# Optimization experiments

Measured on AMD Instinct MI355X. Metric: run time of the kernel, lower is better.

## Reference

```python
import jax, jax.numpy as jnp
import numpy as np

B, IN, H = 4096, 512, 1024
ALPHA, RHO = 0.001, 0.05

def setup_inputs() -> dict:
    key = jax.random.key(0)
    ks = jax.random.split(key, 9)
    inp = jax.random.normal(ks[0], (B, IN), dtype=jnp.float32)
    time = jax.random.uniform(ks[1], (B, 1), dtype=jnp.float32) * 100.0
    hx = jax.random.normal(ks[2], (B, H), dtype=jnp.float32)
    cx = jax.random.normal(ks[3], (B, H), dtype=jnp.float32)
    # params (match torch init scales loosely)
    Wxh_w = jax.random.normal(ks[4], (4 * H, IN), dtype=jnp.float32) / np.sqrt(IN)
    Wxh_b = jnp.zeros((4 * H,), dtype=jnp.float32)
    Whh_w = jax.random.normal(ks[5], (4 * H, H), dtype=jnp.float32) / np.sqrt(H)
    tau = jax.random.normal(ks[6], (H,), dtype=jnp.float32) * 0.5 + 5.0
    s = jax.random.uniform(ks[7], (H,), dtype=jnp.float32) * tau
    alpha = jnp.array([ALPHA], dtype=jnp.float32)
    rho = jnp.array([RHO], dtype=jnp.float32)
    return {"input": inp, "time": time, "hx": hx, "cx": cx,
            "Wxh_w": Wxh_w, "Wxh_b": Wxh_b, "Whh_w": Whh_w,
            "tau": tau, "s": s, "alpha": alpha, "rho": rho}

def _time_gate(time, s, tau, alpha, rho):
    # phi: [B, H] (time [B,1] broadcast against s/tau [H])
    phi = jnp.fmod(time - s, tau) / tau
    k = jnp.where(phi < rho / 2.0, 2.0 * phi / rho,
        jnp.where(phi < rho, 2.0 - 2.0 * phi / rho, alpha * phi))
    # computed under torch.no_grad() in the original
    return jax.lax.stop_gradient(k)

def reference(input, time, hx, cx, Wxh_w, Wxh_b, Whh_w, tau, s, alpha, rho):
    gates = input @ Wxh_w.T + Wxh_b + hx @ Whh_w.T  # [B, 4H]
    i, f, g, o = jnp.split(gates, 4, axis=1)
    k = _time_gate(time, s, tau, alpha, rho)
    ft = jax.nn.sigmoid(f + 1.0 - k)
    it = jax.nn.sigmoid(i) * k
    gt = jnp.tanh(g) * k
    ot = jax.nn.sigmoid(o) * k
    cy = ft * cx + it * gt
    hy = ot * jnp.tanh(cy)
    return (hy, cy)
```

## Files before the change

### kernel.cpp

```cpp
#include <hip/hip_runtime.h>
#include <hip/hip_bf16.h>

#define AS1 __attribute__((address_space(1)))
#define AS3 __attribute__((address_space(3)))

typedef _Float16 half_t;
typedef __attribute__((ext_vector_type(8))) _Float16 f16x8;
typedef __attribute__((ext_vector_type(4))) float f32x4;

static constexpr int Bsz = 4096;
static constexpr int INs = 512;
static constexpr int Hs  = 1024;
static constexpr int BM  = 128;
static constexpr int BH  = 32;
static constexpr int BK  = 64;

static constexpr size_t XN  = (size_t)Bsz * INs;
static constexpr size_t HXN = (size_t)Bsz * Hs;
static constexpr size_t WXN = (size_t)4 * Hs * INs;
static constexpr size_t WHN = (size_t)4 * Hs * Hs;
static constexpr size_t OFF_X  = 0;
static constexpr size_t OFF_HX = XN;
static constexpr size_t OFF_WX = XN + HXN;
static constexpr size_t OFF_WH = XN + HXN + WXN;
static constexpr size_t TOT    = XN + HXN + WXN + WHN;

__global__ __launch_bounds__(256)
void cvt_kernel(const float* __restrict__ x, const float* __restrict__ hx,
                const float* __restrict__ wx, const float* __restrict__ wh,
                half_t* __restrict__ ws) {
  const size_t nthr = (size_t)gridDim.x * blockDim.x;
  for (size_t i8 = (size_t)blockIdx.x * blockDim.x + threadIdx.x;
       i8 < TOT / 8; i8 += nthr) {
    const size_t e = i8 * 8;
    const float* src; size_t off;
    if (e < OFF_HX)      { src = x;  off = e - OFF_X; }
    else if (e < OFF_WX) { src = hx; off = e - OFF_HX; }
    else if (e < OFF_WH) { src = wx; off = e - OFF_WX; }
    else                 { src = wh; off = e - OFF_WH; }
    const f32x4 a = *(const f32x4*)(src + off);
    const f32x4 b = *(const f32x4*)(src + off + 4);
    f16x8 o;
    o[0] = (half_t)a[0]; o[1] = (half_t)a[1]; o[2] = (half_t)a[2]; o[3] = (half_t)a[3];
    o[4] = (half_t)b[0]; o[5] = (half_t)b[1]; o[6] = (half_t)b[2]; o[7] = (half_t)b[3];
    *(f16x8*)(ws + e) = o;
  }
}

template <bool FROMWS>
__global__ __launch_bounds__(256, 2)
void plstm_gemm(const void* __restrict__ xin_,
                const float* __restrict__ timep,
                const void* __restrict__ hxp_,
                const float* __restrict__ cxp,
                const void* __restrict__ wxh_,
                const float* __restrict__ biasp,
                const void* __restrict__ whh_,
                const float* __restrict__ taup,
                const float* __restrict__ sp,
                const float* __restrict__ alphap,
                const float* __restrict__ rhop,
                float* __restrict__ outp)
{
  __shared__ half_t As[BM * BK];
  __shared__ half_t Bs[BM * BK];

  const int tid  = threadIdx.x;
  const int w    = tid >> 6;
  const int lane = tid & 63;
  const int l15  = lane & 15;
  const int grp  = lane >> 4;

  const int m0 = blockIdx.x * BM;
  const int h0 = blockIdx.y * BH;

  f32x4 acc[2][8] = {};

  const int ldr = tid >> 3;
  const int ldc = tid & 7;

  for (int phase = 0; phase < 2; ++phase) {
    const void* Ap = (phase == 0) ? xin_ : hxp_;
    const void* Wp = (phase == 0) ? wxh_ : whh_;
    const int Ka = (phase == 0) ? INs : Hs;

    for (int k0 = 0; k0 < Ka; k0 += BK) {
      #pragma unroll
      for (int i = 0; i < 4; ++i) {
        const int e    = i * 32 + ldr;
        const int gc8  = ldc ^ (e & 7);
        const int wrow = (e >> 5) * Hs + h0 + (e & 31);
        if (FROMWS) {
          const half_t* ga = (const half_t*)Ap + (size_t)(m0 + e) * Ka + (k0 + gc8 * 8);
          __builtin_amdgcn_global_load_lds((AS1 void*)ga,
                                           (AS3 void*)(As + (e * 8 + ldc) * 8), 16, 0, 0);
          const half_t* gw = (const half_t*)Wp + (size_t)wrow * Ka + (k0 + gc8 * 8);
          __builtin_amdgcn_global_load_lds((AS1 void*)gw,
                                           (AS3 void*)(Bs + (e * 8 + ldc) * 8), 16, 0, 0);
        } else {
          const float* ga = (const float*)Ap + (size_t)(m0 + e) * Ka + (k0 + gc8 * 8);
          const f32x4 a0 = *(const f32x4*)ga, a1 = *(const f32x4*)(ga + 4);
          f16x8 pa;
          pa[0]=(half_t)a0[0]; pa[1]=(half_t)a0[1]; pa[2]=(half_t)a0[2]; pa[3]=(half_t)a0[3];
          pa[4]=(half_t)a1[0]; pa[5]=(half_t)a1[1]; pa[6]=(half_t)a1[2]; pa[7]=(half_t)a1[3];
          *(f16x8*)(As + (e * 8 + ldc) * 8) = pa;
          const float* gw = (const float*)Wp + (size_t)wrow * Ka + (k0 + gc8 * 8);
          const f32x4 b0 = *(const f32x4*)gw, b1 = *(const f32x4*)(gw + 4);
          f16x8 pb;
          pb[0]=(half_t)b0[0]; pb[1]=(half_t)b0[1]; pb[2]=(half_t)b0[2]; pb[3]=(half_t)b0[3];
          pb[4]=(half_t)b1[0]; pb[5]=(half_t)b1[1]; pb[6]=(half_t)b1[2]; pb[7]=(half_t)b1[3];
          *(f16x8*)(Bs + (e * 8 + ldc) * 8) = pb;
        }
      }
      __syncthreads();

      #pragma unroll
      for (int kk = 0; kk < 2; ++kk) {
        const int c8 = (kk * 4 + grp) ^ (l15 & 7);
        f16x8 af[2], bfr[8];
        #pragma unroll
        for (int mt = 0; mt < 2; ++mt) {
          const int e = w * 32 + mt * 16 + l15;
          af[mt] = *(const f16x8*)(As + (e * 8 + c8) * 8);
        }
        #pragma unroll
        for (int nt = 0; nt < 8; ++nt) {
          const int e = nt * 16 + l15;
          bfr[nt] = *(const f16x8*)(Bs + (e * 8 + c8) * 8);
        }
        #pragma unroll
        for (int mt = 0; mt < 2; ++mt)
          #pragma unroll
          for (int nt = 0; nt < 8; ++nt)
            acc[mt][nt] = __builtin_amdgcn_mfma_f32_16x16x32_f16(
                af[mt], bfr[nt], acc[mt][nt], 0, 0, 0);
      }
      __syncthreads();
    }
  }

  const float alphav = alphap[0];
  const float rhov   = rhop[0];
  const float rho_half = rhov * 0.5f;

  float sv[2], tauv[2], bi[2], bff[2], bg[2], bo[2];
  #pragma unroll
  for (int nt2 = 0; nt2 < 2; ++nt2) {
    const int h = h0 + nt2 * 16 + l15;
    sv[nt2]   = sp[h];
    tauv[nt2] = taup[h];
    bi[nt2]   = biasp[h];
    bff[nt2]  = biasp[Hs + h];
    bg[nt2]   = biasp[2 * Hs + h];
    bo[nt2]   = biasp[3 * Hs + h];
  }

  #pragma unroll
  for (int mt = 0; mt < 2; ++mt) {
    #pragma unroll
    for (int r = 0; r < 4; ++r) {
      const int brow = m0 + w * 32 + mt * 16 + grp * 4 + r;
      const float timev = timep[brow];
      #pragma unroll
      for (int nt2 = 0; nt2 < 2; ++nt2) {
        const int h = h0 + nt2 * 16 + l15;
        const float iv = acc[mt][0 + nt2][r] + bi[nt2];
        const float fv = acc[mt][2 + nt2][r] + bff[nt2];
        const float gv = acc[mt][4 + nt2][r] + bg[nt2];
        const float ov = acc[mt][6 + nt2][r] + bo[nt2];

        const float phi = fmodf(timev - sv[nt2], tauv[nt2]) / tauv[nt2];
        float kv;
        if (phi < rho_half)      kv = (2.0f * phi) / rhov;
        else if (phi < rhov)     kv = 2.0f - (2.0f * phi) / rhov;
        else                     kv = alphav * phi;

        const float cxv = cxp[(size_t)brow * Hs + h];
        const float ft = 1.0f / (1.0f + expf(-(fv + 1.0f - kv)));
        const float it = kv / (1.0f + expf(-iv));
        const float gt = tanhf(gv) * kv;
        const float ot = kv / (1.0f + expf(-ov));
        const float cy = ft * cxv + it * gt;
        const float hy = ot * tanhf(cy);

        outp[(size_t)brow * Hs + h] = hy;
        outp[(size_t)Bsz * Hs + (size_t)brow * Hs + h] = cy;
      }
    }
  }
}

extern "C" void kernel_launch(void* const* d_in, const int* in_sizes, int n_in,
                              void* d_out, int out_size, void* d_ws, size_t ws_size,
                              hipStream_t stream) {
  (void)in_sizes; (void)n_in; (void)out_size;
  const float* xin   = (const float*)d_in[0];
  const float* timep = (const float*)d_in[1];
  const float* hxp   = (const float*)d_in[2];
  const float* cxp   = (const float*)d_in[3];
  const float* wxh   = (const float*)d_in[4];
  const float* biasp = (const float*)d_in[5];
  const float* whh   = (const float*)d_in[6];
  const float* taup  = (const float*)d_in[7];
  const float* sp    = (const float*)d_in[8];
  const float* alphap= (const float*)d_in[9];
  const float* rhop  = (const float*)d_in[10];
  float* outp = (float*)d_out;

  dim3 grid(Bsz / BM, Hs / BH);
  if (ws_size >= TOT * sizeof(half_t)) {
    half_t* ws = (half_t*)d_ws;
    cvt_kernel<<<2048, 256, 0, stream>>>(xin, hxp, wxh, whh, ws);
    plstm_gemm<true><<<grid, 256, 0, stream>>>(
        ws + OFF_X, timep, ws + OFF_HX, cxp, ws + OFF_WX, biasp, ws + OFF_WH,
        taup, sp, alphap, rhop, outp);
  } else {
    plstm_gemm<false><<<grid, 256, 0, stream>>>(
        xin, timep, hxp, cxp, wxh, biasp, whh,
        taup, sp, alphap, rhop, outp);
  }
}
```

Measured before the change: 203.2 us.

## Rebalance warp tiling, precompute time gate in convert kernel, use fast transcendentals

```diff
diff --git a/kernel.cpp b/kernel.cpp
--- a/kernel.cpp
+++ b/kernel.cpp
@@ -1,5 +1,4 @@
 #include <hip/hip_runtime.h>
-#include <hip/hip_bf16.h>
 
 #define AS1 __attribute__((address_space(1)))
 #define AS3 __attribute__((address_space(3)))
@@ -24,15 +23,26 @@
 static constexpr size_t OFF_WX = XN + HXN;
 static constexpr size_t OFF_WH = XN + HXN + WXN;
 static constexpr size_t TOT    = XN + HXN + WXN + WHN;
+static constexpr size_t KN     = (size_t)Bsz * Hs;
+
+__device__ __forceinline__ float sigm(float x) {
+  return 1.0f / (1.0f + __expf(-x));
+}
+__device__ __forceinline__ float tanh_fast(float x) {
+  const float e = __expf(2.0f * x);
+  return 1.0f - 2.0f / (e + 1.0f);
+}
 
 __global__ __launch_bounds__(256)
 void cvt_kernel(const float* __restrict__ x, const float* __restrict__ hx,
                 const float* __restrict__ wx, const float* __restrict__ wh,
-                half_t* __restrict__ ws) {
-  const size_t nthr = (size_t)gridDim.x * blockDim.x;
-  for (size_t i8 = (size_t)blockIdx.x * blockDim.x + threadIdx.x;
-       i8 < TOT / 8; i8 += nthr) {
-    const size_t e = i8 * 8;
+                const float* __restrict__ timep, const float* __restrict__ sp,
+                const float* __restrict__ taup, const float* __restrict__ alphap,
+                const float* __restrict__ rhop,
+                half_t* __restrict__ ws, float* __restrict__ kout) {
+  const size_t cid = (size_t)blockIdx.x * 256 + threadIdx.x;
+  if (cid < TOT / 8) {
+    const size_t e = cid * 8;
     const float* src; size_t off;
     if (e < OFF_HX)      { src = x;  off = e - OFF_X; }
     else if (e < OFF_WX) { src = hx; off = e - OFF_HX; }
@@ -41,14 +51,38 @@
     const f32x4 a = *(const f32x4*)(src + off);
     const f32x4 b = *(const f32x4*)(src + off + 4);
     f16x8 o;
-    o[0] = (half_t)a[0]; o[1] = (half_t)a[1]; o[2] = (half_t)a[2]; o[3] = (half_t)a[3];
-    o[4] = (half_t)b[0]; o[5] = (half_t)b[1]; o[6] = (half_t)b[2]; o[7] = (half_t)b[3];
+    o[0]=(half_t)a[0]; o[1]=(half_t)a[1]; o[2]=(half_t)a[2]; o[3]=(half_t)a[3];
+    o[4]=(half_t)b[0]; o[5]=(half_t)b[1]; o[6]=(half_t)b[2]; o[7]=(half_t)b[3];
     *(f16x8*)(ws + e) = o;
-  }
-}
-
-template <bool FROMWS>
-__global__ __launch_bounds__(256, 2)
+  } else {
+    const size_t e2 = (cid - TOT / 8) * 8;
+    const int b = (int)(e2 >> 10);
+    const int h = (int)(e2 & 1023);
+    const float tv = timep[b];
+    const float alphav = alphap[0];
+    const float rhov   = rhop[0];
+    const float rh     = 0.5f * rhov;
+    const f32x4 s0 = *(const f32x4*)(sp + h),   s1 = *(const f32x4*)(sp + h + 4);
+    const f32x4 t0 = *(const f32x4*)(taup + h), t1 = *(const f32x4*)(taup + h + 4);
+    f32x4 k0, k1;
+    #pragma unroll
+    for (int j = 0; j < 8; ++j) {
+      const float sv   = j < 4 ? s0[j] : s1[j - 4];
+      const float tauv = j < 4 ? t0[j] : t1[j - 4];
+      const float phi = fmodf(tv - sv, tauv) / tauv;
+      float kv;
+      if (phi < rh)        kv = (2.0f * phi) / rhov;
+      else if (phi < rhov) kv = 2.0f - (2.0f * phi) / rhov;
+      else                 kv = alphav * phi;
+      if (j < 4) k0[j] = kv; else k1[j - 4] = kv;
+    }
+    *(f32x4*)(kout + e2) = k0;
+    *(f32x4*)(kout + e2 + 4) = k1;
+  }
+}
+
+template <int MODE>
+__global__ __launch_bounds__(256, 3)
 void plstm_gemm(const void* __restrict__ xin_,
                 const float* __restrict__ timep,
                 const void* __restrict__ hxp_,
@@ -60,6 +94,7 @@
                 const float* __restrict__ sp,
                 const float* __restrict__ alphap,
                 const float* __restrict__ rhop,
+                const float* __restrict__ kp,
                 float* __restrict__ outp)
 {
   __shared__ half_t As[BM * BK];
@@ -70,11 +105,13 @@
   const int lane = tid & 63;
   const int l15  = lane & 15;
   const int grp  = lane >> 4;
+  const int wr   = w >> 1;
+  const int wc   = w & 1;
 
   const int m0 = blockIdx.x * BM;
   const int h0 = blockIdx.y * BH;
 
-  f32x4 acc[2][8] = {};
+  f32x4 acc[4][4] = {};
 
   const int ldr = tid >> 3;
   const int ldc = tid & 7;
@@ -89,8 +126,8 @@
       for (int i = 0; i < 4; ++i) {
         const int e    = i * 32 + ldr;
         const int gc8  = ldc ^ (e & 7);
-        const int wrow = (e >> 5) * Hs + h0 + (e & 31);
-        if (FROMWS) {
+        const int wrow = ((e >> 4) & 3) * Hs + h0 + ((e >> 6) << 4) + (e & 15);
+        if (MODE >= 1) {
           const half_t* ga = (const half_t*)Ap + (size_t)(m0 + e) * Ka + (k0 + gc8 * 8);
           __builtin_amdgcn_global_load_lds((AS1 void*)ga,
                                            (AS3 void*)(As + (e * 8 + ldc) * 8), 16, 0, 0);
@@ -116,22 +153,22 @@
 
       #pragma unroll
       for (int kk = 0; kk < 2; ++kk) {
-        const int c8 = (kk * 4 + grp) ^ (l15 & 7);
-        f16x8 af[2], bfr[8];
+        const int c8x = (kk * 4 + grp);
+        f16x8 af[4], bfr[4];
         #pragma unroll
-        for (int mt = 0; mt < 2; ++mt) {
-          const int e = w * 32 + mt * 16 + l15;
-          af[mt] = *(const f16x8*)(As + (e * 8 + c8) * 8);
+        for (int mt = 0; mt < 4; ++mt) {
+          const int e = wr * 64 + mt * 16 + l15;
+          af[mt] = *(const f16x8*)(As + (e * 8 + (c8x ^ (l15 & 7))) * 8);
         }
         #pragma unroll
-        for (int nt = 0; nt < 8; ++nt) {
-          const int e = nt * 16 + l15;
-          bfr[nt] = *(const f16x8*)(Bs + (e * 8 + c8) * 8);
+        for (int nt = 0; nt < 4; ++nt) {
+          const int e = wc * 64 + nt * 16 + l15;
+          bfr[nt] = *(const f16x8*)(Bs + (e * 8 + (c8x ^ (l15 & 7))) * 8);
         }
         #pragma unroll
-        for (int mt = 0; mt < 2; ++mt)
+        for (int mt = 0; mt < 4; ++mt)
           #pragma unroll
-          for (int nt = 0; nt < 8; ++nt)
+          for (int nt = 0; nt < 4; ++nt)
             acc[mt][nt] = __builtin_amdgcn_mfma_f32_16x16x32_f16(
                 af[mt], bfr[nt], acc[mt][nt], 0, 0, 0);
       }
@@ -139,53 +176,48 @@
     }
   }
 
-  const float alphav = alphap[0];
-  const float rhov   = rhop[0];
-  const float rho_half = rhov * 0.5f;
-
-  float sv[2], tauv[2], bi[2], bff[2], bg[2], bo[2];
+  const int h = h0 + wc * 16 + l15;
+  const float bi  = biasp[h];
+  const float bfv = biasp[Hs + h];
+  const float bg  = biasp[2 * Hs + h];
+  const float bo  = biasp[3 * Hs + h];
+
+  float sv = 0.f, tauv = 1.f, alphav = 0.f, rhov = 1.f, rh = 0.f;
+  if (MODE < 2) {
+    sv = sp[h]; tauv = taup[h];
+    alphav = alphap[0]; rhov = rhop[0]; rh = 0.5f * rhov;
+  }
+
   #pragma unroll
-  for (int nt2 = 0; nt2 < 2; ++nt2) {
-    const int h = h0 + nt2 * 16 + l15;
-    sv[nt2]   = sp[h];
-    tauv[nt2] = taup[h];
-    bi[nt2]   = biasp[h];
-    bff[nt2]  = biasp[Hs + h];
-    bg[nt2]   = biasp[2 * Hs + h];
-    bo[nt2]   = biasp[3 * Hs + h];
-  }
-
-  #pragma unroll
-  for (int mt = 0; mt < 2; ++mt) {
+  for (int mt = 0; mt < 4; ++mt) {
     #pragma unroll
     for (int r = 0; r < 4; ++r) {
-      const int brow = m0 + w * 32 + mt * 16 + grp * 4 + r;
-      const float timev = timep[brow];
-      #pragma unroll
-      for (int nt2 = 0; nt2 < 2; ++nt2) {
-        const int h = h0 + nt2 * 16 + l15;
-        const float iv = acc[mt][0 + nt2][r] + bi[nt2];
-        const float fv = acc[mt][2 + nt2][r] + bff[nt2];
-        const float gv = acc[mt][4 + nt2][r] + bg[nt2];
-        const float ov = acc[mt][6 + nt2][r] + bo[nt2];
-
-        const float phi = fmodf(timev - sv[nt2], tauv[nt2]) / tauv[nt2];
-        float kv;
-        if (phi < rho_half)      kv = (2.0f * phi) / rhov;
-        else if (phi < rhov)     kv = 2.0f - (2.0f * phi) / rhov;
-        else                     kv = alphav * phi;
-
-        const float cxv = cxp[(size_t)brow * Hs + h];
-        const float ft = 1.0f / (1.0f + expf(-(fv + 1.0f - kv)));
-        const float it = kv / (1.0f + expf(-iv));
-        const float gt = tanhf(gv) * kv;
-        const float ot = kv / (1.0f + expf(-ov));
-        const float cy = ft * cxv + it * gt;
-        const float hy = ot * tanhf(cy);
-
-        outp[(size_t)brow * Hs + h] = hy;
-        outp[(size_t)Bsz * Hs + (size_t)brow * Hs + h] = cy;
+      const int brow = m0 + wr * 64 + mt * 16 + grp * 4 + r;
+      float kv;
+      if (MODE == 2) {
+        kv = kp[(size_t)brow * Hs + h];
+      } else {
+        const float tv = timep[brow];
+        const float phi = fmodf(tv - sv, tauv) / tauv;
+        if (phi < rh)        kv = (2.0f * phi) / rhov;
+        else if (phi < rhov) kv = 2.0f - (2.0f * phi) / rhov;
+        else                 kv = alphav * phi;
       }
+      const float iv = acc[mt][0][r] + bi;
+      const float fv = acc[mt][1][r] + bfv;
+      const float gv = acc[mt][2][r] + bg;
+      const float ov = acc[mt][3][r] + bo;
+
+      const float cxv = cxp[(size_t)brow * Hs + h];
+      const float ft = sigm(fv + 1.0f - kv);
+      const float it = sigm(iv) * kv;
+      const float gt = tanh_fast(gv) * kv;
+      const float ot = sigm(ov) * kv;
+      const float cy = ft * cxv + it * gt;
+      const float hy = ot * tanh_fast(cy);
+
+      outp[(size_t)brow * Hs + h] = hy;
+      outp[(size_t)Bsz * Hs + (size_t)brow * Hs + h] = cy;
     }
   }
 }
@@ -208,15 +240,30 @@
   float* outp = (float*)d_out;
 
   dim3 grid(Bsz / BM, Hs / BH);
-  if (ws_size >= TOT * sizeof(half_t)) {
+  const bool wsF16 = ws_size >= TOT * sizeof(half_t);
+  const bool wsK   = ws_size >= TOT * sizeof(half_t) + KN * sizeof(float);
+
+  if (wsK) {
     half_t* ws = (half_t*)d_ws;
-    cvt_kernel<<<2048, 256, 0, stream>>>(xin, hxp, wxh, whh, ws);
-    plstm_gemm<true><<<grid, 256, 0, stream>>>(
+    float* kout = (float*)(ws + TOT);
+    const int nchunk = (int)(TOT / 8 + KN / 8);
+    cvt_kernel<<<nchunk / 256, 256, 0, stream>>>(xin, hxp, wxh, whh,
+                                                 timep, sp, taup, alphap, rhop,
+                                                 ws, kout);
+    plstm_gemm<2><<<grid, 256, 0, stream>>>(
         ws + OFF_X, timep, ws + OFF_HX, cxp, ws + OFF_WX, biasp, ws + OFF_WH,
-        taup, sp, alphap, rhop, outp);
+        taup, sp, alphap, rhop, kout, outp);
+  } else if (wsF16) {
+    half_t* ws = (half_t*)d_ws;
+    cvt_kernel<<<(int)(TOT / 8 / 256), 256, 0, stream>>>(xin, hxp, wxh, whh,
+                                                 timep, sp, taup, alphap, rhop,
+                                                 ws, nullptr);
+    plstm_gemm<1><<<grid, 256, 0, stream>>>(
+        ws + OFF_X, timep, ws + OFF_HX, cxp, ws + OFF_WX, biasp, ws + OFF_WH,
+        taup, sp, alphap, rhop, nullptr, outp);
   } else {
-    plstm_gemm<false><<<grid, 256, 0, stream>>>(
+    plstm_gemm<0><<<grid, 256, 0, stream>>>(
         xin, timep, hxp, cxp, wxh, biasp, whh,
-        taup, sp, alphap, rhop, outp);
-  }
-}
+        taup, sp, alphap, rhop, nullptr, outp);
+  }
+}
```

Measured after the change: 206.0 us. Within noise of the previous version (+1.4%).
